# Kernel tuning notes

Hardware: AMD Instinct MI355X
Metric: run time of the kernel (lower is better)

The kernel has to match this reference:

```python
import jax, jax.numpy as jnp
import numpy as np

N_NODES = 50000


def _gcn_conv(x, W, b, src, dst, n):
    """PyG GCNConv: add self-loops, symmetric normalization, sum-aggregate."""
    h = x @ W  # [N, out_dim] dense transform first (out_dim <= in_dim path)
    loop = jnp.arange(n, dtype=src.dtype)
    src_sl = jnp.concatenate([src, loop])
    dst_sl = jnp.concatenate([dst, loop])
    # degree computed on destination nodes (incl. self-loops)
    deg = jax.ops.segment_sum(jnp.ones_like(dst_sl, dtype=h.dtype), dst_sl, num_segments=n)
    dinv = jnp.where(deg > 0, jax.lax.rsqrt(deg), 0.0)
    norm = dinv[src_sl] * dinv[dst_sl]  # [E+N]
    msgs = h[src_sl] * norm[:, None]  # gather + scale, [E+N, out_dim]
    out = jax.ops.segment_sum(msgs, dst_sl, num_segments=n)  # scatter-add
    return out + b


def setup_inputs() -> dict:
    key = jax.random.key(0)
    k0, k1, k2, k3 = jax.random.split(key, 4)
    d = 256
    E = 400000
    scale = 1.0 / np.sqrt(d)
    x = jax.random.normal(k0, (N_NODES, d), dtype=jnp.float32)
    edge_index = jax.random.randint(k1, (2, E), 0, N_NODES, dtype=jnp.int64)
    W1 = jax.random.normal(k2, (d, d), dtype=jnp.float32) * scale
    b1 = jnp.zeros((d,), dtype=jnp.float32)
    W2 = jax.random.normal(k3, (d, d), dtype=jnp.float32) * scale
    b2 = jnp.zeros((d,), dtype=jnp.float32)
    return {"x": x, "edge_index": edge_index, "W1": W1, "b1": b1, "W2": W2, "b2": b2}


def reference(x, edge_index, W1, b1, W2, b2):
    src, dst = edge_index[0], edge_index[1]
    h = _gcn_conv(x, W1, b1, src, dst, N_NODES)
    h = jax.nn.relu(h)
    h = _gcn_conv(h, W2, b2, src, dst, N_NODES)
    h = jax.nn.relu(h)
    return h
```

## Files before the change

kernel.cpp:

```cpp
#include <hip/hip_runtime.h>
#include <stdint.h>

typedef __bf16 bf16_t;
typedef bf16_t bf16x4 __attribute__((ext_vector_type(4)));
typedef bf16_t bf16x8 __attribute__((ext_vector_type(8)));
typedef float f32x4 __attribute__((ext_vector_type(4)));

#define DIM 256
#define NNODES 50000

__device__ __forceinline__ int detect_f64(const int* __restrict__ ei) {
    int v = ei[2 * (threadIdx.x & 63) + 1];
    unsigned long long m = __ballot(v == 0);
    return __popcll(m) > 32;
}

__device__ __forceinline__ int load_edge(const int* __restrict__ ei, int E, int f64,
                                         int which , int e) {
    int v = f64 ? ei[(size_t)which * 2 * E + 2 * (size_t)e]
                : ei[(size_t)which * E + (size_t)e];
    return min(max(v, 0), NNODES - 1);
}

__global__ __launch_bounds__(256) void prep_kernel(int* __restrict__ counts,
                                                   const float* __restrict__ W1,
                                                   const float* __restrict__ W2,
                                                   bf16_t* __restrict__ Wf1,
                                                   bf16_t* __restrict__ Wf2, int n) {
    const int nb = (NNODES + 255) / 256;
    int b = blockIdx.x, t = threadIdx.x;
    if (b < nb) {
        int idx = b * 256 + t;
        if (idx < n) counts[idx] = 0;
    } else {
        int cw = b - nb;
        const float* W = (cw & 256) ? W2 : W1;
        bf16_t* Wf = (cw & 256) ? Wf2 : Wf1;
        int k = cw & 255;
        int s = k >> 5, quad = (k >> 3) & 3, j = k & 7;
        int nt = t >> 4, m = t & 15;
        Wf[s * 8192 + (nt * 64 + quad * 16 + m) * 8 + j] = (bf16_t)W[k * DIM + t];
    }
}

__global__ void hist_kernel(const int* __restrict__ ei, int E, int* __restrict__ counts) {
    int f64 = detect_f64(ei);
    int e = blockIdx.x * blockDim.x + threadIdx.x;
    if (e < E) atomicAdd(&counts[load_edge(ei, E, f64, 1, e)], 1);
}

__global__ __launch_bounds__(256) void scan_kernel(const int* __restrict__ counts,
                                                   int* __restrict__ offsets,
                                                   int* __restrict__ cursor,
                                                   float* __restrict__ dinv, int n) {
    __shared__ int red[256];
    __shared__ int sm[256];
    int b = blockIdx.x, t = threadIdx.x;

    int part = 0;
    const int4* c4 = (const int4*)counts;
    int lim = b * 64;
    for (int j = t; j < lim; j += 256) {
        int4 v = c4[j];
        part += v.x + v.y + v.z + v.w;
    }
    red[t] = part;
    __syncthreads();
    #pragma unroll
    for (int off = 128; off > 0; off >>= 1) {
        if (t < off) red[t] += red[t + off];
        __syncthreads();
    }
    int base = red[0];

    int idx = b * 256 + t;
    int v = (idx < n) ? counts[idx] : 0;
    sm[t] = v;
    __syncthreads();
    #pragma unroll
    for (int off = 1; off < 256; off <<= 1) {
        int u = (t >= off) ? sm[t - off] : 0;
        __syncthreads();
        sm[t] += u;
        __syncthreads();
    }
    if (idx < n) {
        int incl = base + sm[t];
        offsets[idx + 1] = incl;
        cursor[idx] = incl - v;
        dinv[idx] = rsqrtf((float)(v + 1));
    }
    if (idx == 0) offsets[0] = 0;
}

template <bool F32A>
__device__ __forceinline__ void gemm_body(const void* __restrict__ Xv,
                                          const bf16_t* __restrict__ Wf,
                                          bf16_t* __restrict__ H, int tiles, int bid,
                                          bf16_t* sB) {
    int tid = threadIdx.x;
    int wave = tid >> 6, lane = tid & 63;
    int m = lane & 15, quad = lane >> 4;
    int t0 = (bid * 4 + wave) * 2;
    int t1 = t0 + 1;
    bool act0 = t0 < tiles, act1 = t1 < tiles;
    int ar0 = min(t0, tiles - 1) * 16 + m;
    int ar1 = min(t1, tiles - 1) * 16 + m;

    f32x4 acc0[16] = {}, acc1[16] = {};

    for (int s = 0; s < 8; s++) {
        __syncthreads();
        {
            const bf16x8* g = (const bf16x8*)Wf + s * 1024;
            bf16x8* d = (bf16x8*)sB;
            #pragma unroll
            for (int it = 0; it < 4; it++) d[tid + it * 256] = g[tid + it * 256];
        }
        __syncthreads();

        bf16x8 a0, a1;
        if (F32A) {
            const f32x4* xp0 = (const f32x4*)((const float*)Xv + (size_t)ar0 * DIM + s * 32 + quad * 8);
            const f32x4* xp1 = (const f32x4*)((const float*)Xv + (size_t)ar1 * DIM + s * 32 + quad * 8);
            f32x4 x0 = xp0[0], x1 = xp0[1], y0 = xp1[0], y1 = xp1[1];
            #pragma unroll
            for (int j = 0; j < 4; j++) {
                a0[j] = (bf16_t)x0[j]; a0[j + 4] = (bf16_t)x1[j];
                a1[j] = (bf16_t)y0[j]; a1[j + 4] = (bf16_t)y1[j];
            }
        } else {
            a0 = *(const bf16x8*)((const bf16_t*)Xv + (size_t)ar0 * DIM + s * 32 + quad * 8);
            a1 = *(const bf16x8*)((const bf16_t*)Xv + (size_t)ar1 * DIM + s * 32 + quad * 8);
        }

        #pragma unroll
        for (int nt = 0; nt < 16; nt++) {
            bf16x8 b = *(const bf16x8*)(sB + nt * 512 + lane * 8);
            acc0[nt] = __builtin_amdgcn_mfma_f32_16x16x32_bf16(a0, b, acc0[nt], 0, 0, 0);
            acc1[nt] = __builtin_amdgcn_mfma_f32_16x16x32_bf16(a1, b, acc1[nt], 0, 0, 0);
        }
    }

    if (act0) {
        int rowb = t0 * 16 + quad * 4;
        #pragma unroll
        for (int nt = 0; nt < 16; nt++) {
            #pragma unroll
            for (int r = 0; r < 4; r++) {
                H[(size_t)(rowb + r) * DIM + nt * 16 + m] = (bf16_t)acc0[nt][r];
            }
        }
    }
    if (act1) {
        int rowb = t1 * 16 + quad * 4;
        #pragma unroll
        for (int nt = 0; nt < 16; nt++) {
            #pragma unroll
            for (int r = 0; r < 4; r++) {
                H[(size_t)(rowb + r) * DIM + nt * 16 + m] = (bf16_t)acc1[nt][r];
            }
        }
    }
}

__global__ __launch_bounds__(256, 3) void gemm1_scatter_kernel(const float* __restrict__ X,
                                                               const bf16_t* __restrict__ Wf,
                                                               bf16_t* __restrict__ H, int tiles,
                                                               int gemm_blocks,
                                                               const int* __restrict__ ei, int E,
                                                               const float* __restrict__ dinv,
                                                               int* __restrict__ cursor,
                                                               int2* __restrict__ csr_e) {
    __shared__ bf16_t sB[8192];
    if ((int)blockIdx.x >= gemm_blocks) {
        int f64 = detect_f64(ei);
        int e = (blockIdx.x - gemm_blocks) * 256 + threadIdx.x;
        if (e < E) {
            int s = load_edge(ei, E, f64, 0, e);
            int d = load_edge(ei, E, f64, 1, e);
            int pos = atomicAdd(&cursor[d], 1);
            if (pos >= 0 && pos < E) {
                int2 v;
                v.x = s;
                v.y = __float_as_int(dinv[s] * dinv[d]);
                csr_e[pos] = v;
            }
        }
        return;
    }
    gemm_body<true>(X, Wf, H, tiles, blockIdx.x, sB);
}

__global__ __launch_bounds__(256, 3) void gemm2_kernel(const bf16_t* __restrict__ Xv,
                                                       const bf16_t* __restrict__ Wf,
                                                       bf16_t* __restrict__ H, int tiles) {
    __shared__ bf16_t sB[8192];
    gemm_body<false>(Xv, Wf, H, tiles, blockIdx.x, sB);
}


template <int OUT_BF16>
__global__ __launch_bounds__(256) void aggregate_kernel(const bf16_t* __restrict__ H,
                                                        const int* __restrict__ offsets,
                                                        const int2* __restrict__ csr_e,
                                                        const float* __restrict__ dinv,
                                                        const float* __restrict__ bias,
                                                        void* __restrict__ outv, int n) {
    int wg = threadIdx.x >> 5;
    int l = threadIdx.x & 31;
    int i = blockIdx.x * 8 + wg;
    if (i >= n) return;

    const char* Hb = (const char*)H;
    int doff = l * 16;

    auto cvt = [](bf16x4 v) -> f32x4 {
        f32x4 r;
        #pragma unroll
        for (int j = 0; j < 4; j++) r[j] = (float)v[j];
        return r;
    };
    auto lo4 = [](bf16x8 v) -> bf16x4 { return __builtin_shufflevector(v, v, 0, 1, 2, 3); };
    auto hi4 = [](bf16x8 v) -> bf16x4 { return __builtin_shufflevector(v, v, 4, 5, 6, 7); };

    float dii = dinv[i];
    bf16x8 selfv = *(const bf16x8*)(Hb + ((size_t)i << 9) + doff);
    f32x4 acc0 = cvt(lo4(selfv)) * (dii * dii);
    f32x4 acc1 = cvt(hi4(selfv)) * (dii * dii);

    int e0 = offsets[i], e1 = offsets[i + 1];
    int e = e0;
    for (; e + 8 <= e1; e += 8) {
        unsigned s[8]; float w[8];
        #pragma unroll
        for (int j = 0; j < 8; j++) {
            int2 t = csr_e[e + j];
            s[j] = min((unsigned)t.x, (unsigned)(NNODES - 1));
            w[j] = __int_as_float(t.y);
        }
        bf16x8 h[8];
        #pragma unroll
        for (int j = 0; j < 8; j++) {
            h[j] = *(const bf16x8*)(Hb + ((size_t)s[j] << 9) + doff);
        }
        __builtin_amdgcn_sched_barrier(0);
        #pragma unroll
        for (int j = 0; j < 8; j++) {
            acc0 += cvt(lo4(h[j])) * w[j];
            acc1 += cvt(hi4(h[j])) * w[j];
        }
    }
    if (e < e1) {
        bf16x8 z;
        #pragma unroll
        for (int q = 0; q < 8; q++) z[q] = (bf16_t)0.0f;
        unsigned s[8]; float w[8]; bool val[8];
        #pragma unroll
        for (int j = 0; j < 8; j++) {
            bool valid = (e + j) < e1;
            val[j] = valid;
            int2 t = csr_e[valid ? e + j : e];
            s[j] = min((unsigned)t.x, (unsigned)(NNODES - 1));
            w[j] = valid ? __int_as_float(t.y) : 0.0f;
        }
        bf16x8 h[8];
        #pragma unroll
        for (int j = 0; j < 8; j++) {
            h[j] = z;
            if (val[j]) h[j] = *(const bf16x8*)(Hb + ((size_t)s[j] << 9) + doff);
        }
        __builtin_amdgcn_sched_barrier(0);
        #pragma unroll
        for (int j = 0; j < 8; j++) {
            acc0 += cvt(lo4(h[j])) * w[j];
            acc1 += cvt(hi4(h[j])) * w[j];
        }
    }

    const f32x4* bp = (const f32x4*)(bias + l * 8);
    acc0 += bp[0];
    acc1 += bp[1];
    #pragma unroll
    for (int j = 0; j < 4; j++) {
        acc0[j] = fmaxf(acc0[j], 0.0f);
        acc1[j] = fmaxf(acc1[j], 0.0f);
    }

    if (OUT_BF16) {
        bf16x8 o;
        #pragma unroll
        for (int j = 0; j < 4; j++) { o[j] = (bf16_t)acc0[j]; o[j + 4] = (bf16_t)acc1[j]; }
        *(bf16x8*)((bf16_t*)outv + (size_t)i * DIM + l * 8) = o;
    } else {
        float* op = (float*)outv + (size_t)i * DIM + l * 8;
        *(f32x4*)op = acc0;
        *(f32x4*)(op + 4) = acc1;
    }
}


extern "C" void kernel_launch(void* const* d_in, const int* in_sizes, int n_in,
                              void* d_out, int out_size, void* d_ws, size_t ws_size,
                              hipStream_t stream) {
    const float* x  = (const float*)d_in[0];
    const int*   ei = (const int*)d_in[1];
    const float* W1 = (const float*)d_in[2];
    const float* b1 = (const float*)d_in[3];
    const float* W2 = (const float*)d_in[4];
    const float* b2 = (const float*)d_in[5];
    float* out = (float*)d_out;

    const int n = NNODES;
    const int E = in_sizes[1] / 2;
    const int nb = (n + 255) / 256;

    char* ws = (char*)d_ws;
    size_t off = 0;
    auto alloc = [&](size_t bytes) -> char* {
        char* p = ws + off;
        off += (bytes + 255) & ~(size_t)255;
        return p;
    };
    float*  dinv     = (float*)alloc((size_t)n * 4);
    int*    counts   = (int*)alloc((size_t)n * 4);
    int*    offsets  = (int*)alloc((size_t)(n + 1) * 4);
    int*    cursor   = (int*)alloc((size_t)n * 4);
    int2*   csr_e    = (int2*)alloc((size_t)E * 8);
    bf16_t* Wf1      = (bf16_t*)alloc((size_t)DIM * DIM * 2);
    bf16_t* Wf2      = (bf16_t*)alloc((size_t)DIM * DIM * 2);
    bf16_t* P        = (bf16_t*)alloc((size_t)n * DIM * 2);
    bf16_t* X2       = (bf16_t*)alloc((size_t)n * DIM * 2);

    int tiles = (n + 15) / 16;
    int pairs = (tiles + 1) / 2;
    int gemm_blocks = (pairs + 3) / 4;
    int hist_blocks = (E + 255) / 256;
    int agg_blocks = (n + 7) / 8;

    prep_kernel<<<nb + 512, 256, 0, stream>>>(counts, W1, W2, Wf1, Wf2, n);
    hist_kernel<<<hist_blocks, 256, 0, stream>>>(ei, E, counts);
    scan_kernel<<<nb, 256, 0, stream>>>(counts, offsets, cursor, dinv, n);
    gemm1_scatter_kernel<<<gemm_blocks + hist_blocks, 256, 0, stream>>>(
        x, Wf1, P, tiles, gemm_blocks, ei, E, dinv, cursor, csr_e);
    aggregate_kernel<1><<<agg_blocks, 256, 0, stream>>>(P, offsets, csr_e, dinv, b1, X2, n);
    gemm2_kernel<<<gemm_blocks, 256, 0, stream>>>(X2, Wf2, P, tiles);
    aggregate_kernel<0><<<agg_blocks, 256, 0, stream>>>(P, offsets, csr_e, dinv, b2, out, n);
}
```

Before: 252.4 us.

## Make GEMM persistent with half of W resident in LDS, split scatter out

The GEMM becomes a persistent kernel on a 256x2 grid. Each block loads one 128-column half of the reordered bf16 weight matrix into 64KB of LDS once, then grid-strides over 16-row tiles. This replaces reloading 8KB weight slices each k-step behind two barriers, and the weight prepack layout changes to match. The CSR edge scatter that used to share a launch with GEMM1 now runs as its own kernel. In exchange, the X tile is read twice (once per column half), each tile carries less MFMA work, and the larger LDS footprint limits occupancy to two blocks.

```diff
diff --git a/kernel.cpp b/kernel.cpp
--- a/kernel.cpp
+++ b/kernel.cpp
@@ -39,7 +39,9 @@
         int k = cw & 255;
         int s = k >> 5, quad = (k >> 3) & 3, j = k & 7;
         int nt = t >> 4, m = t & 15;
-        Wf[s * 8192 + (nt * 64 + quad * 16 + m) * 8 + j] = (bf16_t)W[k * DIM + t];
+        int half = nt >> 3, nt7 = nt & 7;
+        Wf[half * 32768 + s * 4096 + nt7 * 512 + (quad * 16 + m) * 8 + j] =
+            (bf16_t)W[k * DIM + t];
     }
 }
 
@@ -93,112 +95,79 @@
     if (idx == 0) offsets[0] = 0;
 }
 
+__global__ void scatter_kernel(const int* __restrict__ ei, int E,
+                               const float* __restrict__ dinv, int* __restrict__ cursor,
+                               int2* __restrict__ csr_e) {
+    int f64 = detect_f64(ei);
+    int e = blockIdx.x * blockDim.x + threadIdx.x;
+    if (e < E) {
+        int s = load_edge(ei, E, f64, 0, e);
+        int d = load_edge(ei, E, f64, 1, e);
+        int pos = atomicAdd(&cursor[d], 1);
+        if (pos >= 0 && pos < E) {
+            int2 v;
+            v.x = s;
+            v.y = __float_as_int(dinv[s] * dinv[d]);
+            csr_e[pos] = v;
+        }
+    }
+}
+
+
 template <bool F32A>
-__device__ __forceinline__ void gemm_body(const void* __restrict__ Xv,
-                                          const bf16_t* __restrict__ Wf,
-                                          bf16_t* __restrict__ H, int tiles, int bid,
-                                          bf16_t* sB) {
+__global__ __launch_bounds__(256, 2) void gemm_kernel(const void* __restrict__ Xv,
+                                                      const bf16_t* __restrict__ Wf,
+                                                      bf16_t* __restrict__ H, int tiles) {
+    __shared__ bf16_t sB[32768];
     int tid = threadIdx.x;
+    int half = blockIdx.y;
+
+    {
+        const bf16x8* g = (const bf16x8*)(Wf + half * 32768);
+        bf16x8* d = (bf16x8*)sB;
+        #pragma unroll
+        for (int it = 0; it < 16; it++) d[tid + it * 256] = g[tid + it * 256];
+    }
+    __syncthreads();
+
     int wave = tid >> 6, lane = tid & 63;
     int m = lane & 15, quad = lane >> 4;
-    int t0 = (bid * 4 + wave) * 2;
-    int t1 = t0 + 1;
-    bool act0 = t0 < tiles, act1 = t1 < tiles;
-    int ar0 = min(t0, tiles - 1) * 16 + m;
-    int ar1 = min(t1, tiles - 1) * 16 + m;
-
-    f32x4 acc0[16] = {}, acc1[16] = {};
-
-    for (int s = 0; s < 8; s++) {
-        __syncthreads();
-        {
-            const bf16x8* g = (const bf16x8*)Wf + s * 1024;
-            bf16x8* d = (bf16x8*)sB;
+    int wid = blockIdx.x * 4 + wave;
+    int hbase = half * 128;
+
+    for (int tile = wid; tile < tiles; tile += 1024) {
+        int arow = tile * 16 + m;
+        f32x4 acc[8] = {};
+
+        #pragma unroll
+        for (int s = 0; s < 8; s++) {
+            bf16x8 a;
+            if (F32A) {
+                const f32x4* xp = (const f32x4*)((const float*)Xv + (size_t)arow * DIM + s * 32 + quad * 8);
+                f32x4 x0 = xp[0], x1 = xp[1];
+                #pragma unroll
+                for (int j = 0; j < 4; j++) { a[j] = (bf16_t)x0[j]; a[j + 4] = (bf16_t)x1[j]; }
+            } else {
+                a = *(const bf16x8*)((const bf16_t*)Xv + (size_t)arow * DIM + s * 32 + quad * 8);
+            }
+            const bf16_t* bs = sB + s * 4096;
             #pragma unroll
-            for (int it = 0; it < 4; it++) d[tid + it * 256] = g[tid + it * 256];
-        }
-        __syncthreads();
-
-        bf16x8 a0, a1;
-        if (F32A) {
-            const f32x4* xp0 = (const f32x4*)((const float*)Xv + (size_t)ar0 * DIM + s * 32 + quad * 8);
-            const f32x4* xp1 = (const f32x4*)((const float*)Xv + (size_t)ar1 * DIM + s * 32 + quad * 8);
-            f32x4 x0 = xp0[0], x1 = xp0[1], y0 = xp1[0], y1 = xp1[1];
-            #pragma unroll
-            for (int j = 0; j < 4; j++) {
-                a0[j] = (bf16_t)x0[j]; a0[j + 4] = (bf16_t)x1[j];
-                a1[j] = (bf16_t)y0[j]; a1[j + 4] = (bf16_t)y1[j];
+            for (int nt = 0; nt < 8; nt++) {
+                bf16x8 b = *(const bf16x8*)(bs + nt * 512 + lane * 8);
+                acc[nt] = __builtin_amdgcn_mfma_f32_16x16x32_bf16(a, b, acc[nt], 0, 0, 0);
             }
-        } else {
-            a0 = *(const bf16x8*)((const bf16_t*)Xv + (size_t)ar0 * DIM + s * 32 + quad * 8);
-            a1 = *(const bf16x8*)((const bf16_t*)Xv + (size_t)ar1 * DIM + s * 32 + quad * 8);
-        }
-
-        #pragma unroll
-        for (int nt = 0; nt < 16; nt++) {
-            bf16x8 b = *(const bf16x8*)(sB + nt * 512 + lane * 8);
-            acc0[nt] = __builtin_amdgcn_mfma_f32_16x16x32_bf16(a0, b, acc0[nt], 0, 0, 0);
-            acc1[nt] = __builtin_amdgcn_mfma_f32_16x16x32_bf16(a1, b, acc1[nt], 0, 0, 0);
-        }
-    }
-
-    if (act0) {
-        int rowb = t0 * 16 + quad * 4;
-        #pragma unroll
-        for (int nt = 0; nt < 16; nt++) {
+        }
+
+        int rowb = tile * 16 + quad * 4;
+        #pragma unroll
+        for (int nt = 0; nt < 8; nt++) {
             #pragma unroll
             for (int r = 0; r < 4; r++) {
-                H[(size_t)(rowb + r) * DIM + nt * 16 + m] = (bf16_t)acc0[nt][r];
+                H[(size_t)(rowb + r) * DIM + hbase + nt * 16 + m] = (bf16_t)acc[nt][r];
             }
         }
     }
-    if (act1) {
-        int rowb = t1 * 16 + quad * 4;
-        #pragma unroll
-        for (int nt = 0; nt < 16; nt++) {
-            #pragma unroll
-            for (int r = 0; r < 4; r++) {
-                H[(size_t)(rowb + r) * DIM + nt * 16 + m] = (bf16_t)acc1[nt][r];
-            }
-        }
-    }
-}
-
-__global__ __launch_bounds__(256, 3) void gemm1_scatter_kernel(const float* __restrict__ X,
-                                                               const bf16_t* __restrict__ Wf,
-                                                               bf16_t* __restrict__ H, int tiles,
-                                                               int gemm_blocks,
-                                                               const int* __restrict__ ei, int E,
-                                                               const float* __restrict__ dinv,
-                                                               int* __restrict__ cursor,
-                                                               int2* __restrict__ csr_e) {
-    __shared__ bf16_t sB[8192];
-    if ((int)blockIdx.x >= gemm_blocks) {
-        int f64 = detect_f64(ei);
-        int e = (blockIdx.x - gemm_blocks) * 256 + threadIdx.x;
-        if (e < E) {
-            int s = load_edge(ei, E, f64, 0, e);
-            int d = load_edge(ei, E, f64, 1, e);
-            int pos = atomicAdd(&cursor[d], 1);
-            if (pos >= 0 && pos < E) {
-                int2 v;
-                v.x = s;
-                v.y = __float_as_int(dinv[s] * dinv[d]);
-                csr_e[pos] = v;
-            }
-        }
-        return;
-    }
-    gemm_body<true>(X, Wf, H, tiles, blockIdx.x, sB);
-}
-
-__global__ __launch_bounds__(256, 3) void gemm2_kernel(const bf16_t* __restrict__ Xv,
-                                                       const bf16_t* __restrict__ Wf,
-                                                       bf16_t* __restrict__ H, int tiles) {
-    __shared__ bf16_t sB[8192];
-    gemm_body<false>(Xv, Wf, H, tiles, blockIdx.x, sB);
-}
-
+}
 
 template <int OUT_BF16>
 __global__ __launch_bounds__(256) void aggregate_kernel(const bf16_t* __restrict__ H,
@@ -333,17 +302,16 @@
     bf16_t* X2       = (bf16_t*)alloc((size_t)n * DIM * 2);
 
     int tiles = (n + 15) / 16;
-    int pairs = (tiles + 1) / 2;
-    int gemm_blocks = (pairs + 3) / 4;
     int hist_blocks = (E + 255) / 256;
     int agg_blocks = (n + 7) / 8;
+    dim3 gemm_grid(256, 2);
 
     prep_kernel<<<nb + 512, 256, 0, stream>>>(counts, W1, W2, Wf1, Wf2, n);
     hist_kernel<<<hist_blocks, 256, 0, stream>>>(ei, E, counts);
     scan_kernel<<<nb, 256, 0, stream>>>(counts, offsets, cursor, dinv, n);
-    gemm1_scatter_kernel<<<gemm_blocks + hist_blocks, 256, 0, stream>>>(
-        x, Wf1, P, tiles, gemm_blocks, ei, E, dinv, cursor, csr_e);
+    scatter_kernel<<<hist_blocks, 256, 0, stream>>>(ei, E, dinv, cursor, csr_e);
+    gemm_kernel<true><<<gemm_grid, 256, 0, stream>>>(x, Wf1, P, tiles);
     aggregate_kernel<1><<<agg_blocks, 256, 0, stream>>>(P, offsets, csr_e, dinv, b1, X2, n);
-    gemm2_kernel<<<gemm_blocks, 256, 0, stream>>>(X2, Wf2, P, tiles);
+    gemm_kernel<false><<<gemm_grid, 256, 0, stream>>>(X2, Wf2, P, tiles);
     aggregate_kernel<0><<<agg_blocks, 256, 0, stream>>>(P, offsets, csr_e, dinv, b2, out, n);
 }
```

After: 310.9 us. 23.1% more time.
